# Optimization experiments

Hardware: AMD Instinct MI355X
Metric: run time of the kernel (lower is better)

The kernel has to match this reference:

```python
import jax, jax.numpy as jnp
import numpy as np

K = 16                 # nn_k neighbors (self excluded)
FILTER_SCALE = 2.0
SHARPNESS_SIGMA = 0.75
EPS = 1e-17


def _eps_denom(x):
    return jnp.where(x < EPS, EPS, x)


def _normalize(x):
    # F.normalize(dim=-1) semantics
    return x / jnp.maximum(jnp.linalg.norm(x, axis=-1, keepdims=True), 1e-12)


def _gather(feat, idx):
    # feat: (B,P,D), idx: (B,P,K) -> (B,P,K,D)   (== pytorch3d knn_gather)
    return jnp.take_along_axis(feat[:, None, :, :], idx[:, :, :, None], axis=2)


def _knn(points, k):
    # points: (B,P,3) -> squared dists (B,P,k), idxs (B,P,k); self excluded
    d2 = jnp.sum(points * points, axis=-1)
    dists = d2[:, :, None] + d2[:, None, :] - 2.0 * jnp.einsum('bpd,bqd->bpq', points, points)
    P = points.shape[1]
    r = jnp.arange(P)
    dists = dists.at[:, r, r].set(-jnp.inf)  # force self to be rank-0 of top_k
    neg, idx = jax.lax.top_k(-dists, k + 1)
    return jnp.maximum(-neg[:, :, 1:], 0.0), idx[:, :, 1:]


def _denoise(normals, idx, w):
    # weighted neighbor average of normals, per _denoise_normals
    nn_n = _gather(normals, idx)                       # (B,P,K,3)
    return jnp.sum(nn_n * w[..., None], axis=-2) / _eps_denom(
        jnp.sum(w, axis=-1, keepdims=True))


def setup_inputs() -> dict:
    key = jax.random.key(0)
    kp, kn = jax.random.split(key)
    B, P = 2, 8192
    points = jax.random.normal(kp, (B, P, 3), dtype=jnp.float32)
    normals = jax.random.normal(kn, (B, P, 3), dtype=jnp.float32)
    return {"points": points, "normals": normals}


def reference(points, normals):
    # --- torch.no_grad block: knn build + all weights + normal denoising ---
    pts_ng = jax.lax.stop_gradient(points)
    dists, idx = _knn(pts_ng, K)                       # (B,P,K)
    nn = _gather(pts_ng, idx)                          # (B,P,K,3), detached

    # phi = (1 - d/(2*d1*fs^2))^4, clamped at 0 (get_phi)
    s = dists[:, :, :1] * 2.0 * FILTER_SCALE * FILTER_SCALE
    w = jnp.maximum(1.0 - dists / _eps_denom(s), 0.0)
    phi = (w * w) * (w * w)

    n_ng = jax.lax.stop_gradient(normals)
    n1 = _denoise(n_ng, idx, phi)                      # first denoise with phi

    # normal_w = exp(-||n - ni||^2 / sigma^2) on normalized once-denoised normals
    nn_n = _gather(n1, idx)
    diff = _normalize(nn_n) - _normalize(n1)[:, :, None, :]
    inv_sigma = 1.0 / (SHARPNESS_SIGMA * SHARPNESS_SIGMA)
    normal_w = jnp.exp(-jnp.sum(diff * diff, axis=-1) * inv_sigma)

    # second denoise with phi * normal_w
    n2 = _denoise(n1, idx, phi * normal_w)

    # weights_proj = phi * spatial_w_proj(==1) * normal_w, ball-query masked
    weights_proj = phi * normal_w
    ball_mask = dists > FILTER_SCALE * dists[:, :, :1] * 2.0
    weights_proj = jnp.where(ball_mask, 0.0, weights_proj)
    weights_proj = jax.lax.stop_gradient(weights_proj)

    # --- outside no_grad: gather denoised normals, signed point-to-plane ---
    nn_normals = _gather(n2, idx)                      # (B,P,K,3) (no grad path)
    dist_to_surface = jnp.sum((nn - points[:, :, None, :]) * nn_normals, axis=-1)

    # projection loss: weighted mean of squared point-to-plane distance
    loss = jnp.sum(dist_to_surface * dist_to_surface * weights_proj, axis=-1) / \
        _eps_denom(jnp.sum(weights_proj, axis=-1))     # (B,P)
    return jnp.mean(loss)                              # BaseLoss reduction='mean'
```

## Files before the change

### kernel.cpp

```cpp
#include <hip/hip_runtime.h>
#include <math.h>

#define PP    8192
#define NB    2
#define NPTS  16384
#define KNN   16
#define EPSV  1e-17f
#define CH    128
#define NSUP  16
#define NCELL 4096

#define KEY_BIG 3.0e38f


__device__ __forceinline__ int spread3(int v) {
    return (v & 1) | ((v & 2) << 2) | ((v & 4) << 4) | ((v & 8) << 6);
}

__global__ __launch_bounds__(1024) void sort_kernel(
        const float* __restrict__ pts,
        float4* __restrict__ sorted4,
        int*    __restrict__ perm) {
    __shared__ int lh[NCELL];
    __shared__ int wtot[16];
    const int b = blockIdx.x;
    const int t = threadIdx.x;
    const int lane = t & 63, wid = t >> 6;
    const float* bp = pts + (size_t)b * PP * 3;

    for (int k = t; k < NCELL; k += 1024) lh[k] = 0;
    __syncthreads();

    float px[8], py[8], pz[8];
    int cell[8];
#pragma unroll
    for (int k = 0; k < 8; ++k) {
        const int p = t + k * 1024;
        const float x = bp[p * 3 + 0];
        const float y = bp[p * 3 + 1];
        const float z = bp[p * 3 + 2];
        px[k] = x; py[k] = y; pz[k] = z;
        const int ix = (int)fminf(fmaxf((x + 5.0f) * 1.6f, 0.0f), 15.0f);
        const int iy = (int)fminf(fmaxf((y + 5.0f) * 1.6f, 0.0f), 15.0f);
        const int iz = (int)fminf(fmaxf((z + 5.0f) * 1.6f, 0.0f), 15.0f);
        cell[k] = spread3(ix) | (spread3(iy) << 1) | (spread3(iz) << 2);
        atomicAdd(&lh[cell[k]], 1);
    }
    __syncthreads();

    const int v0 = lh[t * 4 + 0];
    const int v1 = lh[t * 4 + 1];
    const int v2 = lh[t * 4 + 2];
    const int v3 = lh[t * 4 + 3];
    const int s4 = v0 + v1 + v2 + v3;
    int v = s4;
#pragma unroll
    for (int off = 1; off < 64; off <<= 1) {
        int uu = __shfl_up(v, off, 64);
        if (lane >= off) v += uu;
    }
    if (lane == 63) wtot[wid] = v;
    __syncthreads();
    if (wid == 0) {
        int w = (lane < 16) ? wtot[lane] : 0;
#pragma unroll
        for (int off = 1; off < 16; off <<= 1) {
            int uu = __shfl_up(w, off, 64);
            if (lane >= off) w += uu;
        }
        if (lane < 16) wtot[lane] = w;
    }
    __syncthreads();
    const int wbase = (wid > 0) ? wtot[wid - 1] : 0;
    const int excl = wbase + v - s4;
    lh[t * 4 + 0] = excl;
    lh[t * 4 + 1] = excl + v0;
    lh[t * 4 + 2] = excl + v0 + v1;
    lh[t * 4 + 3] = excl + v0 + v1 + v2;
    __syncthreads();

#pragma unroll
    for (int k = 0; k < 8; ++k) {
        const int pos = atomicAdd(&lh[cell[k]], 1);
        sorted4[(size_t)b * PP + pos] =
            make_float4(px[k], py[k], pz[k],
                        px[k] * px[k] + py[k] * py[k] + pz[k] * pz[k]);
        perm[b * PP + pos] = t + k * 1024;
    }
}

__global__ void bbox_kernel(const float4* __restrict__ sorted4,
                            float4* __restrict__ bbmin,
                            float4* __restrict__ bbmax,
                            float4* __restrict__ sbmin,
                            float4* __restrict__ sbmax) {
    __shared__ float4 smn[8], smx[8];
    const int lane = threadIdx.x & 63;
    const int wave = threadIdx.x >> 6;
    const int cw = blockIdx.x * 8 + wave;
    const float4 v = sorted4[cw * 64 + lane];
    float mnx = v.x, mny = v.y, mnz = v.z;
    float mxx = v.x, mxy = v.y, mxz = v.z;
#pragma unroll
    for (int off = 32; off >= 1; off >>= 1) {
        mnx = fminf(mnx, __shfl_xor(mnx, off, 64));
        mny = fminf(mny, __shfl_xor(mny, off, 64));
        mnz = fminf(mnz, __shfl_xor(mnz, off, 64));
        mxx = fmaxf(mxx, __shfl_xor(mxx, off, 64));
        mxy = fmaxf(mxy, __shfl_xor(mxy, off, 64));
        mxz = fmaxf(mxz, __shfl_xor(mxz, off, 64));
    }
    if (lane == 0) {
        bbmin[cw] = make_float4(mnx, mny, mnz, 0.f);
        bbmax[cw] = make_float4(mxx, mxy, mxz, 0.f);
        smn[wave] = make_float4(mnx, mny, mnz, 0.f);
        smx[wave] = make_float4(mxx, mxy, mxz, 0.f);
    }
    __syncthreads();
    if (threadIdx.x == 0) {
        float4 a = smn[0], bmx = smx[0];
#pragma unroll
        for (int k = 1; k < 8; ++k) {
            a.x = fminf(a.x, smn[k].x); a.y = fminf(a.y, smn[k].y);
            a.z = fminf(a.z, smn[k].z);
            bmx.x = fmaxf(bmx.x, smx[k].x); bmx.y = fmaxf(bmx.y, smx[k].y);
            bmx.z = fmaxf(bmx.z, smx[k].z);
        }
        sbmin[blockIdx.x] = a;
        sbmax[blockIdx.x] = bmx;
    }
}

__device__ __forceinline__ void insert16(float (&keys)[KNN], float kk) {
#pragma unroll
    for (int s = KNN - 1; s >= 1; --s)
        keys[s] = __builtin_amdgcn_fmed3f(keys[s - 1], kk, keys[s]);
    keys[0] = fminf(keys[0], kk);
}

__device__ __forceinline__ void merge16(float (&a)[KNN], const float (&o)[KNN]) {
    float c[KNN];
#pragma unroll
    for (int s = 0; s < KNN; ++s) c[s] = fminf(a[s], o[KNN - 1 - s]);
#pragma unroll
    for (int st = KNN / 2; st >= 1; st >>= 1) {
#pragma unroll
        for (int base = 0; base < KNN; base += 2 * st) {
#pragma unroll
            for (int k = 0; k < st; ++k) {
                const float x = c[base + k], y = c[base + k + st];
                c[base + k]      = fminf(x, y);
                c[base + k + st] = fmaxf(x, y);
            }
        }
    }
#pragma unroll
    for (int s = 0; s < KNN; ++s) a[s] = c[s];
}

__global__ __launch_bounds__(256) void knn1_kernel(
        const float4* __restrict__ sorted4,
        const int*    __restrict__ perm,
        const float*  __restrict__ normals,
        const float4* __restrict__ bbmin,
        const float4* __restrict__ bbmax,
        const float4* __restrict__ sbmin,
        const float4* __restrict__ sbmax,
        int*   __restrict__ out_idx,
        float* __restrict__ out_phi,
        float* __restrict__ out_n1) {
    const int lane = threadIdx.x & 63;
    const int wv   = threadIdx.x >> 6;
    const int W    = blockIdx.x * 4 + wv;
    const int b    = W >> 13;
    const int qloc = W & (PP - 1);
    const int s0   = qloc >> 9;
    const float4* sb = sorted4 + (size_t)b * PP;
    const int bCH = b * CH;

    const float4 q4 = sb[qloc];
    const float qx = q4.x, qy = q4.y, qz = q4.z;
    const float d2q = qx * qx + qy * qy + qz * qz;

    float keys[KNN];
#pragma unroll
    for (int s = 0; s < KNN; ++s) keys[s] = KEY_BIG;

    auto proc = [&](int c) {
        const int j = c * 64 + lane;
        const float4 c4 = sb[j];
        const float dot = fmaf(qz, c4.z, fmaf(qy, c4.y, qx * c4.x));
        const float d  = fmaf(-2.0f, dot, d2q + c4.w);
        const float dc = fmaxf(d, 0.0f);
        float kv = __uint_as_float(
            (__float_as_uint(dc) & 0xFFFFE000u) | (unsigned)j);
        if (j == qloc) kv = KEY_BIG;
        if (kv < keys[KNN - 1]) insert16(keys, kv);
    };

    const int cb0 = s0 * 8;
    for (int k = 0; k < 8; ++k) proc(cb0 + k);

    unsigned Bq;
    {
        float tk[KNN];
#pragma unroll
        for (int s = 0; s < KNN; ++s) tk[s] = keys[s];
#pragma unroll
        for (int st = 0; st < 5; ++st) {
            const int S = 1 << st;
            float o[KNN];
#pragma unroll
            for (int s = 0; s < KNN; ++s) o[s] = __shfl_xor(tk[s], S, 64);
            merge16(tk, o);
        }
        float o15[KNN];
#pragma unroll
        for (int s = 0; s < KNN; ++s) o15[s] = __shfl_xor(tk[s], 32, 64);
        float B = fminf(tk[0], o15[KNN - 1]);
#pragma unroll
        for (int s = 1; s < KNN; ++s)
            B = fmaxf(B, fminf(tk[s], o15[KNN - 1 - s]));
        Bq = __float_as_uint(B);
    }

    {
        const float4 smn = sbmin[b * NSUP + (lane & 15)];
        const float4 smx = sbmax[b * NSUP + (lane & 15)];
        const float ax = fmaxf(fmaxf(smn.x - qx, qx - smx.x), 0.0f);
        const float ay = fmaxf(fmaxf(smn.y - qy, qy - smx.y), 0.0f);
        const float az = fmaxf(fmaxf(smn.z - qz, qz - smx.z), 0.0f);
        const float dmS = (ax * ax + ay * ay + az * az) * 0.999999f;
        const unsigned flS = __float_as_uint(dmS) & 0xFFFFE000u;
        const unsigned long long M =
            __ballot((lane < 16) && ((lane & 15) != s0) && (flS < Bq));

        for (int s = 0; s < NSUP; ++s) {
            if (!(M & (1ULL << s))) continue;
            const int cc = s * 8 + (lane & 7);
            const float4 cmn = bbmin[bCH + cc];
            const float4 cmx = bbmax[bCH + cc];
            const float bx = fmaxf(fmaxf(cmn.x - qx, qx - cmx.x), 0.0f);
            const float by = fmaxf(fmaxf(cmn.y - qy, qy - cmx.y), 0.0f);
            const float bz = fmaxf(fmaxf(cmn.z - qz, qz - cmx.z), 0.0f);
            const float dmC = (bx * bx + by * by + bz * bz) * 0.999999f;
            const unsigned flC = __float_as_uint(dmC) & 0xFFFFE000u;
            const unsigned long long M2 = __ballot((lane < 8) && (flC < Bq));
#pragma unroll
            for (int k = 0; k < 8; ++k)
                if (M2 & (1ULL << k)) proc(s * 8 + k);
        }
    }

#pragma unroll
    for (int st = 0; st < 6; ++st) {
        const int S = 1 << st;
        float o[KNN];
#pragma unroll
        for (int s = 0; s < KNN; ++s) o[s] = __shfl_xor(keys[s], S, 64);
        merge16(keys, o);
    }

    const int su = lane & 15;
    float myk = keys[0];
#pragma unroll
    for (int s = 1; s < KNN; ++s) myk = (su == s) ? keys[s] : myk;
    const int j = (int)(__float_as_uint(myk) & 0x1FFFu);

    const float4 nb4 = sb[j];
    const float dot = fmaf(qz, nb4.z, fmaf(qy, nb4.y, qx * nb4.x));
    float dd = fmaf(-2.0f, dot, d2q + nb4.w);
    dd = fmaxf(dd, 0.0f);

    float d1 = dd;
#pragma unroll
    for (int st = 0; st < 4; ++st) d1 = fminf(d1, __shfl_xor(d1, 1 << st, 64));

    const float s0v  = d1 * 8.0f;
    const float sden = (s0v < EPSV) ? EPSV : s0v;
    const float w  = fmaxf(1.0f - dd / sden, 0.0f);
    const float ph = (w * w) * (w * w);

    const int qrow = (b << 13) + qloc;
    if (lane < 16) {
        out_idx[qrow * KNN + lane] = j;
        out_phi[qrow * KNN + lane] = ph;
    }

    const float* bn = normals + (size_t)b * PP * 3;
    const int jo = perm[(b << 13) + j];
    const float nx = bn[jo * 3 + 0];
    const float ny = bn[jo * 3 + 1];
    const float nz = bn[jo * 3 + 2];
    float sx = ph * nx, sy = ph * ny, sz = ph * nz, ss = ph;
#pragma unroll
    for (int st = 0; st < 4; ++st) {
        const int S = 1 << st;
        sx += __shfl_xor(sx, S, 64);
        sy += __shfl_xor(sy, S, 64);
        sz += __shfl_xor(sz, S, 64);
        ss += __shfl_xor(ss, S, 64);
    }
    if (lane == 0) {
        const float den = (ss < EPSV) ? EPSV : ss;
        out_n1[qrow * 3 + 0] = sx / den;
        out_n1[qrow * 3 + 1] = sy / den;
        out_n1[qrow * 3 + 2] = sz / den;
    }
}

__global__ __launch_bounds__(256) void denoise2_kernel(
        const int* __restrict__ idx,
        const float* __restrict__ phi,
        const float* __restrict__ n1,
        float* __restrict__ nw_out,
        float* __restrict__ n2_out) {
    const int gid = blockIdx.x * 256 + threadIdx.x;
    const int q = gid >> 4;
    const int s = gid & 15;
    const int b = q >> 13;
    const int gbase = b * PP;
    const float INV_SIG = 1.0f / (0.75f * 0.75f);

    const float ax = n1[q * 3 + 0];
    const float ay = n1[q * 3 + 1];
    const float az = n1[q * 3 + 2];
    const float an = fmaxf(sqrtf(ax * ax + ay * ay + az * az), 1e-12f);
    const float rx = ax / an, ry = ay / an, rz = az / an;

    const int j = idx[q * KNN + s];
    const float bx = n1[(gbase + j) * 3 + 0];
    const float by = n1[(gbase + j) * 3 + 1];
    const float bz = n1[(gbase + j) * 3 + 2];
    const float bnn = fmaxf(sqrtf(bx * bx + by * by + bz * bz), 1e-12f);
    const float ux = bx / bnn - rx;
    const float uy = by / bnn - ry;
    const float uz = bz / bnn - rz;
    const float dq = ux * ux + uy * uy + uz * uz;
    const float nw = expf(-dq * INV_SIG);
    nw_out[q * KNN + s] = nw;

    const float wk = phi[q * KNN + s] * nw;
    float ox = wk * bx, oy = wk * by, oz = wk * bz, swn = wk;
#pragma unroll
    for (int off = 1; off < 16; off <<= 1) {
        ox  += __shfl_xor(ox,  off, 64);
        oy  += __shfl_xor(oy,  off, 64);
        oz  += __shfl_xor(oz,  off, 64);
        swn += __shfl_xor(swn, off, 64);
    }
    if (s == 0) {
        const float den = (swn < EPSV) ? EPSV : swn;
        n2_out[q * 3 + 0] = ox / den;
        n2_out[q * 3 + 1] = oy / den;
        n2_out[q * 3 + 2] = oz / den;
    }
}

__global__ __launch_bounds__(256) void loss_kernel(
        const float4* __restrict__ sorted4,
        const int* __restrict__ idx,
        const float* __restrict__ phi,
        const float* __restrict__ nw,
        const float* __restrict__ n2,
        float* __restrict__ partial) {
    const int gid = blockIdx.x * 256 + threadIdx.x;
    const int q = gid >> 4;
    const int s = gid & 15;
    const int b = q >> 13;
    const int il = q & (PP - 1);
    const float4* sbp = sorted4 + (size_t)b * PP;
    const int gbase = b * PP;

    const float4 p4 = sbp[il];
    const float px = p4.x, py = p4.y, pz = p4.z;
    const float d2q = px * px + py * py + pz * pz;

    const int j = idx[q * KNN + s];
    const float4 nb4 = sbp[j];
    const float dot = fmaf(pz, nb4.z, fmaf(py, nb4.y, px * nb4.x));
    const float dv  = fmaf(-2.0f, dot, d2q + nb4.w);
    const float d   = fmaxf(dv, 0.0f);

    float d1 = d;
#pragma unroll
    for (int off = 1; off < 16; off <<= 1) d1 = fminf(d1, __shfl_xor(d1, off, 64));

    float w = phi[q * KNN + s] * nw[q * KNN + s];
    if (d > 4.0f * d1) w = 0.f;

    const float nx = n2[(gbase + j) * 3 + 0];
    const float ny = n2[(gbase + j) * 3 + 1];
    const float nz = n2[(gbase + j) * 3 + 2];
    const float dts = (nb4.x - px) * nx +
                      (nb4.y - py) * ny +
                      (nb4.z - pz) * nz;
    float num = dts * dts * w, den = w;
#pragma unroll
    for (int off = 1; off < 16; off <<= 1) {
        num += __shfl_xor(num, off, 64);
        den += __shfl_xor(den, off, 64);
    }

    __shared__ float ls[16];
    if (s == 0) {
        const float dd = (den < EPSV) ? EPSV : den;
        ls[threadIdx.x >> 4] = num / dd;
    }
    __syncthreads();
    if (threadIdx.x == 0) {
        float v = 0.f;
#pragma unroll
        for (int k = 0; k < 16; ++k) v += ls[k];
        partial[blockIdx.x] = v;
    }
}

__global__ void finalize_kernel(const float* __restrict__ partial,
                                float* __restrict__ out) {
    float v = 0.f;
#pragma unroll
    for (int k = 0; k < 16; ++k) v += partial[threadIdx.x + 64 * k];
#pragma unroll
    for (int off = 32; off >= 1; off >>= 1) v += __shfl_down(v, off, 64);
    if (threadIdx.x == 0) out[0] = v / (float)NPTS;
}

extern "C" void kernel_launch(void* const* d_in, const int* in_sizes, int n_in,
                              void* d_out, int out_size, void* d_ws, size_t ws_size,
                              hipStream_t stream) {
    const float* points  = (const float*)d_in[0];
    const float* normals = (const float*)d_in[1];
    float* out = (float*)d_out;

    float* wsf    = (float*)d_ws;
    int*   w_idx  = (int*)wsf;
    float* w_phi  = wsf + 262144;
    float* w_nw   = wsf + 524288;
    float* w_n1   = wsf + 786432;
    float* w_n2   = wsf + 835584;
    float4* w_sorted4 = (float4*)(wsf + 884736);
    float* w_part = wsf + 950272;
    int*    w_perm   = (int*)(wsf + 524288);
    float4* w_bbmin  = (float4*)(wsf + 557056);
    float4* w_bbmax  = (float4*)(wsf + 558080);
    float4* w_sbmin  = (float4*)(wsf + 559104);
    float4* w_sbmax  = (float4*)(wsf + 559232);

    sort_kernel   <<<NB, 1024, 0, stream>>>(points, w_sorted4, w_perm);
    bbox_kernel   <<<32, 512, 0, stream>>>(w_sorted4, w_bbmin, w_bbmax,
                                           w_sbmin, w_sbmax);
    knn1_kernel   <<<4096, 256, 0, stream>>>(w_sorted4, w_perm, normals,
                                             w_bbmin, w_bbmax, w_sbmin, w_sbmax,
                                             w_idx, w_phi, w_n1);
    denoise2_kernel<<<1024, 256, 0, stream>>>(w_idx, w_phi, w_n1, w_nw, w_n2);
    loss_kernel   <<<1024, 256, 0, stream>>>(w_sorted4, w_idx, w_phi, w_nw, w_n2, w_part);
    finalize_kernel<<<1, 64, 0, stream>>>(w_part, out);
}
```

Baseline: 139.3 us.

## Seed KNN bound from own 64-point cell via wave bitonic sort

Replaces the initial scan of the query's 8-cell supercell (512 candidates with per-lane top-16 insertion and a multi-round 16-way shuffle merge) with a single 64-candidate cell evaluated one per lane and bitonic-sorted across the wave. The 16th smallest key becomes the pruning bound Bq, and the sorted cell keys are merged into the final result. The own supercell is now traversed like the others, skipping only the own cell, and insertions are also gated by the bound. The bound from 64 candidates is looser than from 512, so more cells may pass the box test, trading cheaper setup for possibly more traversal work.

```diff
diff --git a/kernel.cpp b/kernel.cpp
--- a/kernel.cpp
+++ b/kernel.cpp
@@ -174,13 +174,38 @@
     const int W    = blockIdx.x * 4 + wv;
     const int b    = W >> 13;
     const int qloc = W & (PP - 1);
-    const int s0   = qloc >> 9;
+    const int c0   = qloc >> 6;
     const float4* sb = sorted4 + (size_t)b * PP;
     const int bCH = b * CH;
 
     const float4 q4 = sb[qloc];
     const float qx = q4.x, qy = q4.y, qz = q4.z;
     const float d2q = qx * qx + qy * qy + qz * qz;
+
+    float v;
+    {
+        const int j = c0 * 64 + lane;
+        const float4 c4 = sb[j];
+        const float dot = fmaf(qz, c4.z, fmaf(qy, c4.y, qx * c4.x));
+        const float d  = fmaf(-2.0f, dot, d2q + c4.w);
+        const float dc = fmaxf(d, 0.0f);
+        v = __uint_as_float((__float_as_uint(dc) & 0xFFFFE000u) | (unsigned)j);
+        if (j == qloc) v = KEY_BIG;
+    }
+#pragma unroll
+    for (int kk = 2; kk <= 64; kk <<= 1) {
+#pragma unroll
+        for (int jj = kk >> 1; jj >= 1; jj >>= 1) {
+            const float o = __shfl_xor(v, jj, 64);
+            const bool up    = ((lane & kk) == 0);
+            const bool lower = ((lane & jj) == 0);
+            const float mn = fminf(v, o);
+            const float mx = fmaxf(v, o);
+            v = (lower == up) ? mn : mx;
+        }
+    }
+    const float Bqf = __shfl(v, 15, 64);
+    const unsigned Bq = __float_as_uint(Bqf);
 
     float keys[KNN];
 #pragma unroll
@@ -195,34 +220,8 @@
         float kv = __uint_as_float(
             (__float_as_uint(dc) & 0xFFFFE000u) | (unsigned)j);
         if (j == qloc) kv = KEY_BIG;
-        if (kv < keys[KNN - 1]) insert16(keys, kv);
+        if (kv < fminf(keys[KNN - 1], Bqf)) insert16(keys, kv);
     };
-
-    const int cb0 = s0 * 8;
-    for (int k = 0; k < 8; ++k) proc(cb0 + k);
-
-    unsigned Bq;
-    {
-        float tk[KNN];
-#pragma unroll
-        for (int s = 0; s < KNN; ++s) tk[s] = keys[s];
-#pragma unroll
-        for (int st = 0; st < 5; ++st) {
-            const int S = 1 << st;
-            float o[KNN];
-#pragma unroll
-            for (int s = 0; s < KNN; ++s) o[s] = __shfl_xor(tk[s], S, 64);
-            merge16(tk, o);
-        }
-        float o15[KNN];
-#pragma unroll
-        for (int s = 0; s < KNN; ++s) o15[s] = __shfl_xor(tk[s], 32, 64);
-        float B = fminf(tk[0], o15[KNN - 1]);
-#pragma unroll
-        for (int s = 1; s < KNN; ++s)
-            B = fmaxf(B, fminf(tk[s], o15[KNN - 1 - s]));
-        Bq = __float_as_uint(B);
-    }
 
     {
         const float4 smn = sbmin[b * NSUP + (lane & 15)];
@@ -232,8 +231,7 @@
         const float az = fmaxf(fmaxf(smn.z - qz, qz - smx.z), 0.0f);
         const float dmS = (ax * ax + ay * ay + az * az) * 0.999999f;
         const unsigned flS = __float_as_uint(dmS) & 0xFFFFE000u;
-        const unsigned long long M =
-            __ballot((lane < 16) && ((lane & 15) != s0) && (flS < Bq));
+        const unsigned long long M = __ballot((lane < 16) && (flS < Bq));
 
         for (int s = 0; s < NSUP; ++s) {
             if (!(M & (1ULL << s))) continue;
@@ -247,8 +245,10 @@
             const unsigned flC = __float_as_uint(dmC) & 0xFFFFE000u;
             const unsigned long long M2 = __ballot((lane < 8) && (flC < Bq));
 #pragma unroll
-            for (int k = 0; k < 8; ++k)
-                if (M2 & (1ULL << k)) proc(s * 8 + k);
+            for (int k = 0; k < 8; ++k) {
+                const int c = s * 8 + k;
+                if ((M2 & (1ULL << k)) && c != c0) proc(c);
+            }
         }
     }
 
@@ -259,6 +259,12 @@
 #pragma unroll
         for (int s = 0; s < KNN; ++s) o[s] = __shfl_xor(keys[s], S, 64);
         merge16(keys, o);
+    }
+    {
+        float ck[KNN];
+#pragma unroll
+        for (int s = 0; s < KNN; ++s) ck[s] = __shfl(v, s, 64);
+        merge16(keys, ck);
     }
 
     const int su = lane & 15;
```

New measurement: 143.7 us. 3.2% more time.
